# Kernel tuning notes

Hardware: AMD Instinct MI355X
Metric: run time of the kernel (lower is better)

The kernel has to match this reference:

```python
import jax, jax.numpy as jnp
import numpy as np

K = 5
K2 = K * K  # 25
SLOPE = 0.01  # torch leaky_relu default


def _unfold(x, k):
    # torch.nn.Unfold(k) on reflect-padded x: channel order c-major, then kh, kw
    b, c, h, w = x.shape
    p = k // 2
    xp = jnp.pad(x, ((0, 0), (0, 0), (p, p), (p, p)), mode='reflect')
    cols = jnp.stack([xp[:, :, i:i + h, j:j + w] for i in range(k) for j in range(k)], axis=2)
    return cols.reshape(b, c * k * k, h * w)  # (b, 3*k^2, h*w)


def _lin(x, W, b):
    # torch Linear: W is (out, in)
    return x @ W.T + b


def _lrelu(x):
    return jnp.where(x >= 0, x, SLOPE * x)


def setup_inputs() -> dict:
    key = jax.random.key(0)
    ks = iter(jax.random.split(key, 64))
    d = {}
    d['x'] = jax.random.uniform(next(ks), (4, 3, 384, 384), dtype=jnp.float32)

    def mk(name, out_f, in_f):
        d['W_' + name] = jax.random.normal(next(ks), (out_f, in_f), jnp.float32) * (1.0 / np.sqrt(in_f))
        d['b_' + name] = jax.random.normal(next(ks), (out_f,), jnp.float32) * 0.01

    mk('input', 2 * K2, 3 * K2)
    mk('h1', 3 * K2, 2 * K2)
    mk('h2', 3 * K2, 3 * K2)
    mk('h3', 2 * K2, 2 * K2)
    mk('h4', 5 * K2, 2 * K2)
    mk('h5', 2 * K2, 5 * K2)
    mk('out', 3, 2 * K2)
    # encoder(3*k^2): in -> 3*in -> in -> 3
    mk('e1', 9 * K2, 3 * K2); mk('e2', 3 * K2, 9 * K2); mk('e3', 3, 3 * K2)
    # encoder(2*k^2)
    mk('f1', 6 * K2, 2 * K2); mk('f2', 2 * K2, 6 * K2); mk('f3', 3, 2 * K2)
    # decoder(2*k^2): 3 -> out -> 3*out -> out
    mk('d1', 2 * K2, 3); mk('d2', 6 * K2, 2 * K2); mk('d3', 2 * K2, 6 * K2)
    return d


def reference(x,
              W_input, b_input, W_h1, b_h1, W_h2, b_h2, W_h3, b_h3,
              W_h4, b_h4, W_h5, b_h5, W_out, b_out,
              W_e1, b_e1, W_e2, b_e2, W_e3, b_e3,
              W_f1, b_f1, W_f2, b_f2, W_f3, b_f3,
              W_d1, b_d1, W_d2, b_d2, W_d3, b_d3):
    b, c, h, w = x.shape
    sw = jnp.transpose(_unfold(x, K), (0, 2, 1))  # (b, h*w, 3*k^2)
    x1 = _lin(sw, W_input, b_input)
    x2 = _lrelu(_lin(x1, W_h1, b_h1))
    x3 = jnp.tanh(_lin(x2, W_h2, b_h2))
    x3_enc = _lin(_lin(_lin(x3, W_e1, b_e1), W_e2, b_e2), W_e3, b_e3)
    enc2_x1 = _lin(_lin(_lin(x1, W_f1, b_f1), W_f2, b_f2), W_f3, b_f3)
    x4 = _lrelu(x3_enc + enc2_x1)
    x4_dec = _lin(_lin(_lin(_lin(x4, W_d1, b_d1), W_d2, b_d2), W_d3, b_d3), W_h3, b_h3)
    x5 = jnp.tanh(_lin(x4_dec, W_h4, b_h4))
    x6 = _lin(x5, W_h5, b_h5) - x1
    x7 = _lrelu(_lin(x6, W_out, b_out))  # (b, h*w, 3)
    return jnp.transpose(x7, (0, 2, 1)).reshape(b, c, h, w)
```

## Files before the change

### kernel.cpp

```cpp
#include <hip/hip_runtime.h>


#define IW 384
#define HW (384 * 384)
#define NPIX (4 * HW)
#define MTILE 128
#define NBLK (NPIX / MTILE)
#define NST 52
#define PT16 (16 * NST)

typedef _Float16 half8 __attribute__((ext_vector_type(8)));
typedef __fp16 fp16x2 __attribute__((ext_vector_type(2)));
typedef __attribute__((ext_vector_type(4))) float f32x4;
typedef __attribute__((ext_vector_type(2))) unsigned int uint2_;

#define MFMAH(A, B, C) __builtin_amdgcn_mfma_f32_16x16x32_f16((A), (B), (C), 0, 0, 0)

#define BA   0
#define B1   64
#define B2   144
#define BEF  224
#define BD   240
#define B4   304
#define B5   432
#define BOUT 496
#define BIAS_TOT 512

#define W_A0   0
#define W_A1   2048
#define W_A2   4096
#define W_H1A  6144
#define W_H1B  8704
#define W_H2A  11264
#define W_H2B  13824
#define W_H2C  16384
#define W_EF   18944
#define W_D    24064
#define W_H4C0 28160
#define W_H5C0 30208
#define W_OUT  44544
#define W_NI   45568
#define W_TOT  47616

#define STG_BE  24320
#define STG_BF  24336

__device__ __forceinline__ float lrelu(float v) { return fmaxf(v, 0.01f * v); }

#if __has_builtin(__builtin_amdgcn_exp2f)
#define EXP2F __builtin_amdgcn_exp2f
#else
#define EXP2F __builtin_exp2f
#endif

__device__ __forceinline__ float tanh_fast(float v) {
    float e = EXP2F(v * 2.8853900817779268f);
    return __builtin_fmaf(-2.0f, __builtin_amdgcn_rcpf(e + 1.0f), 1.0f);
}

__device__ __forceinline__ unsigned short f2h_bits(float v) {
    union { _Float16 h; unsigned short s; } u; u.h = (_Float16)v; return u.s;
}
__device__ __forceinline__ float h2f_bits(unsigned short s) {
    union { _Float16 h; unsigned short s; } u; u.s = s; return (float)u.h;
}
__device__ __forceinline__ unsigned packh2(float a, float b) {
    union { fp16x2 h; unsigned u; } u;
    u.h = __builtin_amdgcn_cvt_pkrtz(a, b);
    return u.u;
}

__device__ __forceinline__ void stage(float* dst, const float* __restrict__ src,
                                      int n, int tid) {
    int n4 = n >> 2;
    float4* d = (float4*)dst;
    const float4* s = (const float4*)src;
#pragma unroll 4
    for (int i = tid; i < n4; i += 256) d[i] = s[i];
    for (int i = (n4 << 2) + tid; i < n; i += 256) dst[i] = src[i];
}

__global__ __launch_bounds__(256) void setup_all(
    const float* __restrict__ W_input, const float* __restrict__ b_input,
    const float* __restrict__ W_h1,  const float* __restrict__ b_h1,
    const float* __restrict__ W_h2,  const float* __restrict__ b_h2,
    const float* __restrict__ W_h3,  const float* __restrict__ b_h3,
    const float* __restrict__ W_h4,  const float* __restrict__ b_h4,
    const float* __restrict__ W_h5,  const float* __restrict__ b_h5,
    const float* __restrict__ W_out, const float* __restrict__ b_out,
    const float* __restrict__ W_e1,  const float* __restrict__ b_e1,
    const float* __restrict__ W_e2,  const float* __restrict__ b_e2,
    const float* __restrict__ W_e3,  const float* __restrict__ b_e3,
    const float* __restrict__ W_f1,  const float* __restrict__ b_f1,
    const float* __restrict__ W_f2,  const float* __restrict__ b_f2,
    const float* __restrict__ W_f3,  const float* __restrict__ b_f3,
    const float* __restrict__ W_d1,  const float* __restrict__ b_d1,
    const float* __restrict__ W_d2,  const float* __restrict__ b_d2,
    const float* __restrict__ W_d3,  const float* __restrict__ b_d3,
    float* __restrict__ ws)
{
    const int tid = threadIdx.x;
    const int NT = 256;
    short* wimg = (short*)(ws + BIAS_TOT);

    if (blockIdx.x < 71) {
        const int soff[17] = {W_A0,W_A1,W_A2, W_H1A,W_H1B, W_H2A,W_H2B,W_H2C,
                              W_H4C0,W_H5C0, W_H4C0+4096,W_H5C0+4096,
                              W_H4C0+8192,W_H5C0+8192, W_H4C0+12288,W_H5C0+12288,
                              W_OUT};
        const int slay[17] = {0,0,0, 1,1, 2,2,2, 6,7, 6,7, 6,7, 6,7, 8};
        const int sNT[17]  = {4,4,4, 5,5, 5,5,5, 2,4, 2,4, 2,4, 2,4, 1};
        const int sKTS[17] = {1,1,1, 1,1, 1,1,1, 2,1, 2,1, 2,1, 2,1, 2};
        const int snb[17]  = {0,0,0, 0,0, 0,0,0, 0,0, 32,0, 64,0, 96,0, 0};
        const int skb[17]  = {0,32,64, 0,32, 0,32,64, 0,0, 0,32, 0,64, 0,96, 0};

        int seg = 0, local = blockIdx.x;
        while (seg < 16 && local >= sNT[seg] * sKTS[seg]) { local -= sNT[seg] * sKTS[seg]; seg++; }
        const int kts = sKTS[seg];
        const int kt = local % kts, nt = local / kts;
        const int lay = slay[seg];
        short* dst = wimg + soff[seg] + local * 512;

#pragma unroll
        for (int t = 0; t < 2; t++) {
            int idx = tid + t * 256;
            int j = idx & 7, lane = idx >> 3;
            int n = snb[seg] + nt * 16 + (lane & 15);
            int k = skb[seg] + kt * 32 + (lane >> 4) * 8 + j;
            float v = 0.0f;
            switch (lay) {
                case 0: if (n < 50  && k < 75)  v = W_input[n * 75 + k]; break;
                case 1: if (n < 75  && k < 50)  v = W_h1[n * 50 + k]; break;
                case 2: if (n < 75  && k < 75)  v = W_h2[n * 75 + k]; break;
                case 6: if (n < 125 && k < 50)  v = W_h4[n * 50 + k]; break;
                case 7: if (n < 50  && k < 125) v = W_h5[n * 125 + k]; break;
                case 8: if (n < 3   && k < 50)  v = W_out[n * 50 + k]; break;
            }
            dst[idx] = (short)f2h_bits(v);
        }
        return;
    }

    if (blockIdx.x == 74) {
        for (int i = tid; i < BIAS_TOT; i += NT) {
            if (i >= BD && i < B4) continue;
            float v = 0.0f;
            if (i < B1)        { int o = i - BA;   if (o < 50)  v = b_input[o]; }
            else if (i < B2)   { int o = i - B1;   if (o < 75)  v = b_h1[o]; }
            else if (i < BEF)  { int o = i - B2;   if (o < 75)  v = b_h2[o]; }
            else if (i < BD)   { v = 0.0f; }
            else if (i < B5)   { int o = i - B4;   if (o < 125) v = b_h4[o]; }
            else if (i < BOUT) { int o = i - B5;   if (o < 50)  v = b_h5[o]; }
            else               { int o = i - BOUT; if (o < 3)   v = b_out[o]; }
            ws[i] = v;
        }
        for (int i = tid; i < 2048; i += NT) {
            int j = i & 7, lane = (i >> 3) & 63, nt = i >> 9;
            int n = nt * 16 + (lane & 15);
            int k = (nt >> 1) * 32 + (lane >> 4) * 8 + j;
            wimg[W_NI + i] = (short)f2h_bits(k == n ? -1.0f : 0.0f);
        }
        return;
    }

    __shared__ __align__(16) float A[17500];
    __shared__ float B[675];
    __shared__ float C[256];
    __shared__ float Dd[256];
    __shared__ float Es[256];
    __shared__ float S[232];

    if (blockIdx.x == 71) {
        stage(A, W_e2, 16875, tid);
        for (int i = tid; i < 225; i += NT) { Es[i] = W_e3[i]; C[i] = b_e1[i]; }
        __syncthreads();
        for (int o = tid; o < 675; o += NT) {
            int r = o / 225, c = o % 225;
            float s0 = 0.f, s1 = 0.f, s2 = 0.f;
#pragma unroll
            for (int t = 0; t < 75; t += 3) {
                s0 += Es[r * 75 + t]     * A[t * 225 + c];
                s1 += Es[r * 75 + t + 1] * A[(t + 1) * 225 + c];
                s2 += Es[r * 75 + t + 2] * A[(t + 2) * 225 + c];
            }
            B[o] = s0 + s1 + s2;
        }
        for (int o = tid; o < 75; o += NT) {
            float s0 = 0.f, s1 = 0.f, s2 = 0.f;
#pragma unroll
            for (int t = 0; t < 225; t += 3) {
                s0 += A[o * 225 + t]     * C[t];
                s1 += A[o * 225 + t + 1] * C[t + 1];
                s2 += A[o * 225 + t + 2] * C[t + 2];
            }
            Dd[o] = b_e2[o] + s0 + s1 + s2;
        }
        __syncthreads();
        stage(A, W_e1, 16875, tid);
        __syncthreads();
        for (int o = tid; o < 225; o += NT) {
            int r = o / 75, c = o % 75;
            float s0 = 0.f, s1 = 0.f, s2 = 0.f;
#pragma unroll
            for (int t = 0; t < 225; t += 3) {
                s0 += B[r * 225 + t]     * A[t * 75 + c];
                s1 += B[r * 225 + t + 1] * A[(t + 1) * 75 + c];
                s2 += B[r * 225 + t + 2] * A[(t + 2) * 75 + c];
            }
            S[o] = s0 + s1 + s2;
        }
        for (int o = tid; o < 16; o += NT) {
            float s = 0.0f;
            if (o < 3) {
                s = b_e3[o];
                for (int t = 0; t < 75; t++) s += Es[o * 75 + t] * Dd[t];
            }
            ws[STG_BE + o] = s;
        }
        __syncthreads();
        for (int i = tid; i < 3072; i += NT) {
            int j = i & 7, lane = (i >> 3) & 63, frag = i >> 9, pl = frag & 1, kt = frag >> 1;
            int n = lane & 15, k = kt * 32 + (lane >> 4) * 8 + j;
            float v = (n < 3 && k < 75) ? S[n * 75 + k] : 0.0f;
            float hi = h2f_bits(f2h_bits(v));
            wimg[W_EF + i] = (short)(pl ? f2h_bits(v - hi) : f2h_bits(v));
        }
    } else if (blockIdx.x == 72) {
        stage(A,        W_f2, 7500, tid);
        stage(A + 7500, W_f1, 7500, tid);
        for (int i = tid; i < 150; i += NT) { Es[i] = W_f3[i]; C[i] = b_f1[i]; }
        __syncthreads();
        for (int o = tid; o < 450; o += NT) {
            int r = o / 150, c = o % 150;
            float s0 = 0.f, s1 = 0.f;
#pragma unroll
            for (int t = 0; t < 50; t += 2) {
                s0 += Es[r * 50 + t]     * A[t * 150 + c];
                s1 += Es[r * 50 + t + 1] * A[(t + 1) * 150 + c];
            }
            B[o] = s0 + s1;
        }
        for (int o = tid; o < 50; o += NT) {
            float s0 = 0.f, s1 = 0.f;
#pragma unroll
            for (int t = 0; t < 150; t += 2) {
                s0 += A[o * 150 + t]     * C[t];
                s1 += A[o * 150 + t + 1] * C[t + 1];
            }
            Dd[o] = b_f2[o] + s0 + s1;
        }
        __syncthreads();
        for (int o = tid; o < 150; o += NT) {
            int r = o / 50, c = o % 50;
            float s0 = 0.f, s1 = 0.f;
#pragma unroll
            for (int t = 0; t < 150; t += 2) {
                s0 += B[r * 150 + t]     * A[7500 + t * 50 + c];
                s1 += B[r * 150 + t + 1] * A[7500 + (t + 1) * 50 + c];
            }
            S[o] = s0 + s1;
        }
        for (int o = tid; o < 16; o += NT) {
            float s = 0.0f;
            if (o < 3) {
                s = b_f3[o];
                for (int t = 0; t < 50; t++) s += Es[o * 50 + t] * Dd[t];
            }
            ws[STG_BF + o] = s;
        }
        __syncthreads();
        for (int i = tid; i < 2048; i += NT) {
            int j = i & 7, lane = (i >> 3) & 63, frag = i >> 9, pl = frag & 1, kt = frag >> 1;
            int n = lane & 15, k = kt * 32 + (lane >> 4) * 8 + j;
            float v = (n < 3 && k < 50) ? S[n * 50 + k] : 0.0f;
            float hi = h2f_bits(f2h_bits(v));
            wimg[W_EF + 3072 + i] = (short)(pl ? f2h_bits(v - hi) : f2h_bits(v));
        }
    } else {
        stage(A,         W_d2, 7500, tid);
        stage(A + 7500,  W_d3, 7500, tid);
        stage(A + 15000, W_h3, 2500, tid);
        for (int i = tid; i < 150; i += NT) Es[i] = W_d1[i];
        for (int i = tid; i < 50;  i += NT) C[i] = b_d1[i];
        __syncthreads();
        for (int o = tid; o < 450; o += NT) {
            int r = o / 3, c = o % 3;
            float s0 = 0.f, s1 = 0.f;
#pragma unroll
            for (int t = 0; t < 50; t += 2) {
                s0 += A[r * 50 + t]     * Es[t * 3 + c];
                s1 += A[r * 50 + t + 1] * Es[(t + 1) * 3 + c];
            }
            B[o] = s0 + s1;
        }
        for (int o = tid; o < 150; o += NT) {
            float s0 = 0.f, s1 = 0.f;
#pragma unroll
            for (int t = 0; t < 50; t += 2) {
                s0 += A[o * 50 + t]     * C[t];
                s1 += A[o * 50 + t + 1] * C[t + 1];
            }
            Dd[o] = b_d2[o] + s0 + s1;
        }
        __syncthreads();
        for (int o = tid; o < 150; o += NT) {
            int r = o / 3, c = o % 3;
            float s0 = 0.f, s1 = 0.f;
#pragma unroll
            for (int t = 0; t < 150; t += 2) {
                s0 += A[7500 + r * 150 + t]     * B[t * 3 + c];
                s1 += A[7500 + r * 150 + t + 1] * B[(t + 1) * 3 + c];
            }
            Es[o] = s0 + s1;
        }
        for (int o = tid; o < 50; o += NT) {
            float s0 = 0.f, s1 = 0.f;
#pragma unroll
            for (int t = 0; t < 150; t += 2) {
                s0 += A[7500 + o * 150 + t]     * Dd[t];
                s1 += A[7500 + o * 150 + t + 1] * Dd[t + 1];
            }
            C[o] = b_d3[o] + s0 + s1;
        }
        __syncthreads();
        for (int o = tid; o < 150; o += NT) {
            int r = o / 3, c = o % 3;
            float s0 = 0.f, s1 = 0.f;
#pragma unroll
            for (int t = 0; t < 50; t += 2) {
                s0 += A[15000 + r * 50 + t]     * Es[t * 3 + c];
                s1 += A[15000 + r * 50 + t + 1] * Es[(t + 1) * 3 + c];
            }
            S[o] = s0 + s1;
        }
        for (int o = tid; o < 64; o += NT) {
            float v = 0.0f;
            if (o < 50) {
                float s0 = 0.f, s1 = 0.f;
#pragma unroll
                for (int t = 0; t < 50; t += 2) {
                    s0 += A[15000 + o * 50 + t]     * C[t];
                    s1 += A[15000 + o * 50 + t + 1] * C[t + 1];
                }
                v = b_h3[o] + s0 + s1;
            }
            ws[BD + o] = v;
        }
        __syncthreads();
        for (int i = tid; i < 4096; i += NT) {
            int j = i & 7, lane = (i >> 3) & 63, frag = i >> 9, pl = frag & 1, nt = frag >> 1;
            int n = nt * 16 + (lane & 15), k = (lane >> 4) * 8 + j;
            float v = (n < 50 && k < 3) ? S[n * 3 + k] : 0.0f;
            float hi = h2f_bits(f2h_bits(v));
            wimg[W_D + i] = (short)(pl ? f2h_bits(v - hi) : f2h_bits(v));
        }
    }
}

__device__ __forceinline__ half8 gfragH(const short* __restrict__ wl, int off) {
    return *(const half8*)(wl + off);
}

__device__ __forceinline__ void wB(unsigned int* p, f32x4 v) {
    uint2_ u;
    u[0] = packh2(v[0], v[1]);
    u[1] = packh2(v[2], v[3]);
    *(uint2_*)p = u;
}

__device__ __forceinline__ f32x4 lrelu4(f32x4 v) {
    v[0] = lrelu(v[0]); v[1] = lrelu(v[1]); v[2] = lrelu(v[2]); v[3] = lrelu(v[3]);
    return v;
}
__device__ __forceinline__ f32x4 tanh4(f32x4 v) {
    v[0] = tanh_fast(v[0]); v[1] = tanh_fast(v[1]);
    v[2] = tanh_fast(v[2]); v[3] = tanh_fast(v[3]);
    return v;
}

__global__ __launch_bounds__(256, 4) void fused_mfma(
    const float* __restrict__ xin,
    const float* __restrict__ ws,
    float* __restrict__ out)
{
    __shared__ unsigned int acts[MTILE * NST];

    const int tid = threadIdx.x;
    const int wv = tid >> 6;
    const int lane = tid & 63;
    const int qd = lane >> 4;
    const int mcol = lane & 15;
    const short* __restrict__ wl = (const short*)(ws + BIAS_TOT) + lane * 8;

    const int g0 = blockIdx.x * MTILE;
    const int bb = g0 / HW;
    const int p0 = g0 - bb * HW;
    const int yb = p0 / IW;
    const int xblk = p0 - yb * IW;
    const float* __restrict__ xb = xin + bb * 3 * HW;

    float* patch = (float*)acts;
    int*   stab  = (int*)(acts + 1984);

    for (int e = tid; e < 1980; e += 256) {
        int cr = e / 132;
        int i  = e - cr * 132;
        int c  = cr / 5, r = cr - c * 5;
        int ty = yb + r - 2; ty = ty < 0 ? -ty : ty; ty = (766 - ty) < ty ? 766 - ty : ty;
        int tx = xblk - 2 + i; tx = tx < 0 ? -tx : tx; tx = (766 - tx) < tx ? 766 - tx : tx;
        patch[cr * 132 + i] = xb[c * HW + ty * IW + tx];
    }
    if (tid < 96) {
        int v = 0;
        if (tid < 75) {
            int c = tid / 25, rem = tid - 25 * c;
            int rr = rem / 5, ss = rem - 5 * rr;
            v = (c * 5 + rr) * 132 + ss;
        }
        stab[tid] = v;
    }
    __syncthreads();

    half8 swf[3][2];
    {
        int st[3][8];
#pragma unroll
        for (int kt = 0; kt < 3; kt++)
#pragma unroll
            for (int j = 0; j < 8; j++)
                st[kt][j] = stab[kt * 32 + qd * 8 + j];
#pragma unroll
        for (int pt = 0; pt < 2; pt++) {
            const int xloc = wv * 32 + pt * 16 + mcol;
#pragma unroll
            for (int kt = 0; kt < 3; kt++) {
                union { unsigned u32[4]; half8 v; } u;
#pragma unroll
                for (int jj = 0; jj < 8; jj += 2) {
                    float v0 = patch[st[kt][jj]     + xloc];
                    float v1 = patch[st[kt][jj + 1] + xloc];
                    u.u32[jj >> 1] = packh2(v0, v1);
                }
                swf[kt][pt] = u.v;
            }
        }
    }
    __syncthreads();

    unsigned int* myrow = acts + (wv * 32 + mcol) * NST;
    unsigned int* wp = myrow + 2 * qd;
    const unsigned int* rp = myrow + 4 * qd;

    {
        uint2_ z; z[0] = 0u; z[1] = 0u;
        *(uint2_*)(wp + 40) = z;
        *(uint2_*)(wp + PT16 + 40) = z;
    }

    f32x4 accA[4][2];
#pragma unroll
    for (int mt = 0; mt < 4; mt++) {
        f32x4 b = *(const f32x4*)(ws + BA + mt * 16 + qd * 4);
        accA[mt][0] = b; accA[mt][1] = b;
    }
#pragma unroll
    for (int kt = 0; kt < 3; kt++)
#pragma unroll
        for (int mt = 0; mt < 4; mt++) {
            half8 w = gfragH(wl, W_A0 + kt * 2048 + mt * 512);
            accA[mt][0] = MFMAH(w, swf[kt][0], accA[mt][0]);
            accA[mt][1] = MFMAH(w, swf[kt][1], accA[mt][1]);
        }
#pragma unroll
    for (int mt = 0; mt < 4; mt++) {
        wB(wp + mt * 8,        accA[mt][0]);
        wB(wp + PT16 + mt * 8, accA[mt][1]);
    }
    half8 x1f[2][2];
#pragma unroll
    for (int kt = 0; kt < 2; kt++) {
        x1f[kt][0] = *(const half8*)(rp + kt * 16);
        x1f[kt][1] = *(const half8*)(rp + PT16 + kt * 16);
    }

    f32x4 acc1[5][2];
#pragma unroll
    for (int mt = 0; mt < 5; mt++) {
        f32x4 b = *(const f32x4*)(ws + B1 + mt * 16 + qd * 4);
        acc1[mt][0] = b; acc1[mt][1] = b;
    }
#pragma unroll
    for (int kt = 0; kt < 2; kt++)
#pragma unroll
        for (int mt = 0; mt < 5; mt++) {
            half8 w = gfragH(wl, W_H1A + kt * 2560 + mt * 512);
            acc1[mt][0] = MFMAH(w, x1f[kt][0], acc1[mt][0]);
            acc1[mt][1] = MFMAH(w, x1f[kt][1], acc1[mt][1]);
        }
#pragma unroll
    for (int mt = 0; mt < 5; mt++) {
        wB(wp + mt * 8,        lrelu4(acc1[mt][0]));
        wB(wp + PT16 + mt * 8, lrelu4(acc1[mt][1]));
    }

    f32x4 acc2[5][2];
#pragma unroll
    for (int mt = 0; mt < 5; mt++) {
        f32x4 b = *(const f32x4*)(ws + B2 + mt * 16 + qd * 4);
        acc2[mt][0] = b; acc2[mt][1] = b;
    }
#pragma unroll
    for (int kt = 0; kt < 3; kt++) {
        half8 a0 = *(const half8*)(rp + kt * 16);
        half8 a1 = *(const half8*)(rp + PT16 + kt * 16);
#pragma unroll
        for (int mt = 0; mt < 5; mt++) {
            half8 w = gfragH(wl, W_H2A + kt * 2560 + mt * 512);
            acc2[mt][0] = MFMAH(w, a0, acc2[mt][0]);
            acc2[mt][1] = MFMAH(w, a1, acc2[mt][1]);
        }
    }
#pragma unroll
    for (int mt = 0; mt < 5; mt++) {
        wB(wp + mt * 8,        tanh4(acc2[mt][0]));
        wB(wp + PT16 + mt * 8, tanh4(acc2[mt][1]));
    }

    f32x4 accEF[2];
    {
        f32x4 be = *(const f32x4*)(ws + STG_BE + qd * 4);
        f32x4 bf = *(const f32x4*)(ws + STG_BF + qd * 4);
        f32x4 b = be + bf;
        accEF[0] = b; accEF[1] = b;
    }
#pragma unroll
    for (int kt = 0; kt < 3; kt++) {
        half8 a0 = *(const half8*)(rp + kt * 16);
        half8 a1 = *(const half8*)(rp + PT16 + kt * 16);
        half8 wh = gfragH(wl, W_EF + kt * 1024);
        half8 wo = gfragH(wl, W_EF + kt * 1024 + 512);
        accEF[0] = MFMAH(wh, a0, accEF[0]); accEF[0] = MFMAH(wo, a0, accEF[0]);
        accEF[1] = MFMAH(wh, a1, accEF[1]); accEF[1] = MFMAH(wo, a1, accEF[1]);
    }
#pragma unroll
    for (int kt = 0; kt < 2; kt++) {
        half8 wh = gfragH(wl, W_EF + 3072 + kt * 1024);
        half8 wo = gfragH(wl, W_EF + 3072 + kt * 1024 + 512);
        accEF[0] = MFMAH(wh, x1f[kt][0], accEF[0]); accEF[0] = MFMAH(wo, x1f[kt][0], accEF[0]);
        accEF[1] = MFMAH(wh, x1f[kt][1], accEF[1]); accEF[1] = MFMAH(wo, x1f[kt][1], accEF[1]);
    }
    wB(wp,        lrelu4(accEF[0]));
    wB(wp + PT16, lrelu4(accEF[1]));

    half8 x4f[2];
    x4f[0] = *(const half8*)(rp);
    x4f[1] = *(const half8*)(rp + PT16);
    f32x4 accD[4][2];
#pragma unroll
    for (int mt = 0; mt < 4; mt++) {
        f32x4 b = *(const f32x4*)(ws + BD + mt * 16 + qd * 4);
        accD[mt][0] = b; accD[mt][1] = b;
    }
#pragma unroll
    for (int mt = 0; mt < 4; mt++) {
        half8 wh = gfragH(wl, W_D + mt * 1024);
        half8 wo = gfragH(wl, W_D + mt * 1024 + 512);
        accD[mt][0] = MFMAH(wh, x4f[0], accD[mt][0]); accD[mt][0] = MFMAH(wo, x4f[0], accD[mt][0]);
        accD[mt][1] = MFMAH(wh, x4f[1], accD[mt][1]); accD[mt][1] = MFMAH(wo, x4f[1], accD[mt][1]);
    }
#pragma unroll
    for (int mt = 0; mt < 4; mt++) {
        wB(wp + mt * 8,        accD[mt][0]);
        wB(wp + PT16 + mt * 8, accD[mt][1]);
    }
    half8 xdf[2][2];
#pragma unroll
    for (int kt = 0; kt < 2; kt++) {
        xdf[kt][0] = *(const half8*)(rp + kt * 16);
        xdf[kt][1] = *(const half8*)(rp + PT16 + kt * 16);
    }

    f32x4 x6a[4][2];
#pragma unroll
    for (int mt = 0; mt < 4; mt++) {
        f32x4 b = *(const f32x4*)(ws + B5 + mt * 16 + qd * 4);
        half8 nI = gfragH(wl, W_NI + mt * 512);
        x6a[mt][0] = MFMAH(nI, x1f[mt >> 1][0], b);
        x6a[mt][1] = MFMAH(nI, x1f[mt >> 1][1], b);
    }

#pragma unroll
    for (int c = 0; c < 4; c++) {
        const int slot = (c & 1) ? 16 : 32;
        f32x4 acc5[2][2];
#pragma unroll
        for (int mt2 = 0; mt2 < 2; mt2++) {
            f32x4 b = *(const f32x4*)(ws + B4 + c * 32 + mt2 * 16 + qd * 4);
            acc5[mt2][0] = b; acc5[mt2][1] = b;
        }
#pragma unroll
        for (int kt = 0; kt < 2; kt++)
#pragma unroll
            for (int mt2 = 0; mt2 < 2; mt2++) {
                half8 w = gfragH(wl, W_H4C0 + c * 4096 + (mt2 * 2 + kt) * 512);
                acc5[mt2][0] = MFMAH(w, xdf[kt][0], acc5[mt2][0]);
                acc5[mt2][1] = MFMAH(w, xdf[kt][1], acc5[mt2][1]);
            }
#pragma unroll
        for (int mt2 = 0; mt2 < 2; mt2++) {
            wB(wp + slot + mt2 * 8,        tanh4(acc5[mt2][0]));
            wB(wp + PT16 + slot + mt2 * 8, tanh4(acc5[mt2][1]));
        }
        half8 ch0 = *(const half8*)(rp + slot);
        half8 ch1 = *(const half8*)(rp + PT16 + slot);
#pragma unroll
        for (int mt = 0; mt < 4; mt++) {
            half8 w = gfragH(wl, W_H5C0 + c * 4096 + mt * 512);
            x6a[mt][0] = MFMAH(w, ch0, x6a[mt][0]);
            x6a[mt][1] = MFMAH(w, ch1, x6a[mt][1]);
        }
    }

#pragma unroll
    for (int mt = 0; mt < 4; mt++) {
        wB(wp + mt * 8,        x6a[mt][0]);
        wB(wp + PT16 + mt * 8, x6a[mt][1]);
    }
    f32x4 accO[2];
    {
        f32x4 b = *(const f32x4*)(ws + BOUT + qd * 4);
        accO[0] = b; accO[1] = b;
    }
#pragma unroll
    for (int kt = 0; kt < 2; kt++) {
        half8 a0 = *(const half8*)(rp + kt * 16);
        half8 a1 = *(const half8*)(rp + PT16 + kt * 16);
        half8 w = gfragH(wl, W_OUT + kt * 512);
        accO[0] = MFMAH(w, a0, accO[0]);
        accO[1] = MFMAH(w, a1, accO[1]);
    }
    if (qd == 0) {
#pragma unroll
        for (int pt = 0; pt < 2; pt++) {
            int p = p0 + wv * 32 + pt * 16 + mcol;
#pragma unroll
            for (int r = 0; r < 3; r++)
                out[(bb * 3 + r) * HW + p] = lrelu(accO[pt][r]);
        }
    }
}

extern "C" void kernel_launch(void* const* d_in, const int* in_sizes, int n_in,
                              void* d_out, int out_size, void* d_ws, size_t ws_size,
                              hipStream_t stream)
{
    const float* xin = (const float*)d_in[0];
    float* ws = (float*)d_ws;

    setup_all<<<75, 256, 0, stream>>>(
        (const float*)d_in[1],  (const float*)d_in[2],
        (const float*)d_in[3],  (const float*)d_in[4],
        (const float*)d_in[5],  (const float*)d_in[6],
        (const float*)d_in[7],  (const float*)d_in[8],
        (const float*)d_in[9],  (const float*)d_in[10],
        (const float*)d_in[11], (const float*)d_in[12],
        (const float*)d_in[13], (const float*)d_in[14],
        (const float*)d_in[15], (const float*)d_in[16],
        (const float*)d_in[17], (const float*)d_in[18],
        (const float*)d_in[19], (const float*)d_in[20],
        (const float*)d_in[21], (const float*)d_in[22],
        (const float*)d_in[23], (const float*)d_in[24],
        (const float*)d_in[25], (const float*)d_in[26],
        (const float*)d_in[27], (const float*)d_in[28],
        (const float*)d_in[29], (const float*)d_in[30],
        (const float*)d_in[31], (const float*)d_in[32],
        ws);

    fused_mfma<<<NBLK, 256, 0, stream>>>(xin, ws, (float*)d_out);
}
```

Baseline: 235.6 us.

## Chain MFMA layers in registers by permuting weight K-order instead of LDS round-trips

Stops writing each layer's fp16 activations to a shared-memory staging buffer and reading them back as B fragments. The weight images are prepacked with a permuted K ordering, so the MFMA accumulator output of one layer can be packed directly into the next layer's input fragment in registers. This removes LDS traffic and the associated waits between every layer and shrinks the shared allocation. In exchange it raises register pressure, and the out-of-range K lanes of the first layer now have to be zeroed explicitly.

```diff
diff --git a/kernel.cpp b/kernel.cpp
--- a/kernel.cpp
+++ b/kernel.cpp
@@ -6,13 +6,10 @@
 #define NPIX (4 * HW)
 #define MTILE 128
 #define NBLK (NPIX / MTILE)
-#define NST 52
-#define PT16 (16 * NST)
 
 typedef _Float16 half8 __attribute__((ext_vector_type(8)));
 typedef __fp16 fp16x2 __attribute__((ext_vector_type(2)));
 typedef __attribute__((ext_vector_type(4))) float f32x4;
-typedef __attribute__((ext_vector_type(2))) unsigned int uint2_;
 
 #define MFMAH(A, B, C) __builtin_amdgcn_mfma_f32_16x16x32_f16((A), (B), (C), 0, 0, 0)
 
@@ -125,8 +122,10 @@
         for (int t = 0; t < 2; t++) {
             int idx = tid + t * 256;
             int j = idx & 7, lane = idx >> 3;
+            int slot = (lay == 0) ? ((lane >> 4) * 8 + j)
+                                  : (4 * (lane >> 4) + (j & 3) + 16 * (j >> 2));
             int n = snb[seg] + nt * 16 + (lane & 15);
-            int k = skb[seg] + kt * 32 + (lane >> 4) * 8 + j;
+            int k = skb[seg] + kt * 32 + slot;
             float v = 0.0f;
             switch (lay) {
                 case 0: if (n < 50  && k < 75)  v = W_input[n * 75 + k]; break;
@@ -157,7 +156,7 @@
         for (int i = tid; i < 2048; i += NT) {
             int j = i & 7, lane = (i >> 3) & 63, nt = i >> 9;
             int n = nt * 16 + (lane & 15);
-            int k = (nt >> 1) * 32 + (lane >> 4) * 8 + j;
+            int k = (nt >> 1) * 32 + 4 * (lane >> 4) + (j & 3) + 16 * (j >> 2);
             wimg[W_NI + i] = (short)f2h_bits(k == n ? -1.0f : 0.0f);
         }
         return;
@@ -220,7 +219,8 @@
         __syncthreads();
         for (int i = tid; i < 3072; i += NT) {
             int j = i & 7, lane = (i >> 3) & 63, frag = i >> 9, pl = frag & 1, kt = frag >> 1;
-            int n = lane & 15, k = kt * 32 + (lane >> 4) * 8 + j;
+            int n = lane & 15;
+            int k = kt * 32 + 4 * (lane >> 4) + (j & 3) + 16 * (j >> 2);
             float v = (n < 3 && k < 75) ? S[n * 75 + k] : 0.0f;
             float hi = h2f_bits(f2h_bits(v));
             wimg[W_EF + i] = (short)(pl ? f2h_bits(v - hi) : f2h_bits(v));
@@ -271,7 +271,8 @@
         __syncthreads();
         for (int i = tid; i < 2048; i += NT) {
             int j = i & 7, lane = (i >> 3) & 63, frag = i >> 9, pl = frag & 1, kt = frag >> 1;
-            int n = lane & 15, k = kt * 32 + (lane >> 4) * 8 + j;
+            int n = lane & 15;
+            int k = kt * 32 + 4 * (lane >> 4) + (j & 3) + 16 * (j >> 2);
             float v = (n < 3 && k < 50) ? S[n * 50 + k] : 0.0f;
             float hi = h2f_bits(f2h_bits(v));
             wimg[W_EF + 3072 + i] = (short)(pl ? f2h_bits(v - hi) : f2h_bits(v));
@@ -349,7 +350,8 @@
         __syncthreads();
         for (int i = tid; i < 4096; i += NT) {
             int j = i & 7, lane = (i >> 3) & 63, frag = i >> 9, pl = frag & 1, nt = frag >> 1;
-            int n = nt * 16 + (lane & 15), k = (lane >> 4) * 8 + j;
+            int n = nt * 16 + (lane & 15);
+            int k = 4 * (lane >> 4) + (j & 3) + 16 * (j >> 2);
             float v = (n < 50 && k < 3) ? S[n * 3 + k] : 0.0f;
             float hi = h2f_bits(f2h_bits(v));
             wimg[W_D + i] = (short)(pl ? f2h_bits(v - hi) : f2h_bits(v));
@@ -361,11 +363,20 @@
     return *(const half8*)(wl + off);
 }
 
-__device__ __forceinline__ void wB(unsigned int* p, f32x4 v) {
-    uint2_ u;
-    u[0] = packh2(v[0], v[1]);
-    u[1] = packh2(v[2], v[3]);
-    *(uint2_*)p = u;
+__device__ __forceinline__ half8 packB(f32x4 lo, f32x4 hi) {
+    union { unsigned u32[4]; half8 v; } u;
+    u.u32[0] = packh2(lo[0], lo[1]);
+    u.u32[1] = packh2(lo[2], lo[3]);
+    u.u32[2] = packh2(hi[0], hi[1]);
+    u.u32[3] = packh2(hi[2], hi[3]);
+    return u.v;
+}
+__device__ __forceinline__ half8 packB1(f32x4 lo) {
+    union { unsigned u32[4]; half8 v; } u;
+    u.u32[0] = packh2(lo[0], lo[1]);
+    u.u32[1] = packh2(lo[2], lo[3]);
+    u.u32[2] = 0u; u.u32[3] = 0u;
+    return u.v;
 }
 
 __device__ __forceinline__ f32x4 lrelu4(f32x4 v) {
@@ -383,7 +394,8 @@
     const float* __restrict__ ws,
     float* __restrict__ out)
 {
-    __shared__ unsigned int acts[MTILE * NST];
+    __shared__ float patch[1984];
+    __shared__ int stab[96];
 
     const int tid = threadIdx.x;
     const int wv = tid >> 6;
@@ -398,9 +410,6 @@
     const int yb = p0 / IW;
     const int xblk = p0 - yb * IW;
     const float* __restrict__ xb = xin + bb * 3 * HW;
-
-    float* patch = (float*)acts;
-    int*   stab  = (int*)(acts + 1984);
 
     for (int e = tid; e < 1980; e += 256) {
         int cr = e / 132;
@@ -439,22 +448,16 @@
                 for (int jj = 0; jj < 8; jj += 2) {
                     float v0 = patch[st[kt][jj]     + xloc];
                     float v1 = patch[st[kt][jj + 1] + xloc];
+                    if (kt == 2) {
+                        int qq0 = 64 + qd * 8 + jj;
+                        v0 = (qq0     < 75) ? v0 : 0.0f;
+                        v1 = (qq0 + 1 < 75) ? v1 : 0.0f;
+                    }
                     u.u32[jj >> 1] = packh2(v0, v1);
                 }
                 swf[kt][pt] = u.v;
             }
         }
-    }
-    __syncthreads();
-
-    unsigned int* myrow = acts + (wv * 32 + mcol) * NST;
-    unsigned int* wp = myrow + 2 * qd;
-    const unsigned int* rp = myrow + 4 * qd;
-
-    {
-        uint2_ z; z[0] = 0u; z[1] = 0u;
-        *(uint2_*)(wp + 40) = z;
-        *(uint2_*)(wp + PT16 + 40) = z;
     }
 
     f32x4 accA[4][2];
@@ -471,17 +474,12 @@
             accA[mt][0] = MFMAH(w, swf[kt][0], accA[mt][0]);
             accA[mt][1] = MFMAH(w, swf[kt][1], accA[mt][1]);
         }
-#pragma unroll
-    for (int mt = 0; mt < 4; mt++) {
-        wB(wp + mt * 8,        accA[mt][0]);
-        wB(wp + PT16 + mt * 8, accA[mt][1]);
-    }
     half8 x1f[2][2];
 #pragma unroll
-    for (int kt = 0; kt < 2; kt++) {
-        x1f[kt][0] = *(const half8*)(rp + kt * 16);
-        x1f[kt][1] = *(const half8*)(rp + PT16 + kt * 16);
-    }
+    for (int kt = 0; kt < 2; kt++)
+#pragma unroll
+        for (int pt = 0; pt < 2; pt++)
+            x1f[kt][pt] = packB(accA[2 * kt][pt], accA[2 * kt + 1][pt]);
 
     f32x4 acc1[5][2];
 #pragma unroll
@@ -497,10 +495,12 @@
             acc1[mt][0] = MFMAH(w, x1f[kt][0], acc1[mt][0]);
             acc1[mt][1] = MFMAH(w, x1f[kt][1], acc1[mt][1]);
         }
-#pragma unroll
-    for (int mt = 0; mt < 5; mt++) {
-        wB(wp + mt * 8,        lrelu4(acc1[mt][0]));
-        wB(wp + PT16 + mt * 8, lrelu4(acc1[mt][1]));
+    half8 x2f[3][2];
+#pragma unroll
+    for (int pt = 0; pt < 2; pt++) {
+        x2f[0][pt] = packB (lrelu4(acc1[0][pt]), lrelu4(acc1[1][pt]));
+        x2f[1][pt] = packB (lrelu4(acc1[2][pt]), lrelu4(acc1[3][pt]));
+        x2f[2][pt] = packB1(lrelu4(acc1[4][pt]));
     }
 
     f32x4 acc2[5][2];
@@ -510,20 +510,19 @@
         acc2[mt][0] = b; acc2[mt][1] = b;
     }
 #pragma unroll
-    for (int kt = 0; kt < 3; kt++) {
-        half8 a0 = *(const half8*)(rp + kt * 16);
-        half8 a1 = *(const half8*)(rp + PT16 + kt * 16);
+    for (int kt = 0; kt < 3; kt++)
 #pragma unroll
         for (int mt = 0; mt < 5; mt++) {
             half8 w = gfragH(wl, W_H2A + kt * 2560 + mt * 512);
-            acc2[mt][0] = MFMAH(w, a0, acc2[mt][0]);
-            acc2[mt][1] = MFMAH(w, a1, acc2[mt][1]);
-        }
-    }
-#pragma unroll
-    for (int mt = 0; mt < 5; mt++) {
-        wB(wp + mt * 8,        tanh4(acc2[mt][0]));
-        wB(wp + PT16 + mt * 8, tanh4(acc2[mt][1]));
+            acc2[mt][0] = MFMAH(w, x2f[kt][0], acc2[mt][0]);
+            acc2[mt][1] = MFMAH(w, x2f[kt][1], acc2[mt][1]);
+        }
+    half8 x3f[3][2];
+#pragma unroll
+    for (int pt = 0; pt < 2; pt++) {
+        x3f[0][pt] = packB (tanh4(acc2[0][pt]), tanh4(acc2[1][pt]));
+        x3f[1][pt] = packB (tanh4(acc2[2][pt]), tanh4(acc2[3][pt]));
+        x3f[2][pt] = packB1(tanh4(acc2[4][pt]));
     }
 
     f32x4 accEF[2];
@@ -535,12 +534,10 @@
     }
 #pragma unroll
     for (int kt = 0; kt < 3; kt++) {
-        half8 a0 = *(const half8*)(rp + kt * 16);
-        half8 a1 = *(const half8*)(rp + PT16 + kt * 16);
         half8 wh = gfragH(wl, W_EF + kt * 1024);
         half8 wo = gfragH(wl, W_EF + kt * 1024 + 512);
-        accEF[0] = MFMAH(wh, a0, accEF[0]); accEF[0] = MFMAH(wo, a0, accEF[0]);
-        accEF[1] = MFMAH(wh, a1, accEF[1]); accEF[1] = MFMAH(wo, a1, accEF[1]);
+        accEF[0] = MFMAH(wh, x3f[kt][0], accEF[0]); accEF[0] = MFMAH(wo, x3f[kt][0], accEF[0]);
+        accEF[1] = MFMAH(wh, x3f[kt][1], accEF[1]); accEF[1] = MFMAH(wo, x3f[kt][1], accEF[1]);
     }
 #pragma unroll
     for (int kt = 0; kt < 2; kt++) {
@@ -549,12 +546,11 @@
         accEF[0] = MFMAH(wh, x1f[kt][0], accEF[0]); accEF[0] = MFMAH(wo, x1f[kt][0], accEF[0]);
         accEF[1] = MFMAH(wh, x1f[kt][1], accEF[1]); accEF[1] = MFMAH(wo, x1f[kt][1], accEF[1]);
     }
-    wB(wp,        lrelu4(accEF[0]));
-    wB(wp + PT16, lrelu4(accEF[1]));
-
     half8 x4f[2];
-    x4f[0] = *(const half8*)(rp);
-    x4f[1] = *(const half8*)(rp + PT16);
+#pragma unroll
+    for (int pt = 0; pt < 2; pt++)
+        x4f[pt] = packB1(lrelu4(accEF[pt]));
+
     f32x4 accD[4][2];
 #pragma unroll
     for (int mt = 0; mt < 4; mt++) {
@@ -568,17 +564,12 @@
         accD[mt][0] = MFMAH(wh, x4f[0], accD[mt][0]); accD[mt][0] = MFMAH(wo, x4f[0], accD[mt][0]);
         accD[mt][1] = MFMAH(wh, x4f[1], accD[mt][1]); accD[mt][1] = MFMAH(wo, x4f[1], accD[mt][1]);
     }
-#pragma unroll
-    for (int mt = 0; mt < 4; mt++) {
-        wB(wp + mt * 8,        accD[mt][0]);
-        wB(wp + PT16 + mt * 8, accD[mt][1]);
-    }
     half8 xdf[2][2];
 #pragma unroll
-    for (int kt = 0; kt < 2; kt++) {
-        xdf[kt][0] = *(const half8*)(rp + kt * 16);
-        xdf[kt][1] = *(const half8*)(rp + PT16 + kt * 16);
-    }
+    for (int kt = 0; kt < 2; kt++)
+#pragma unroll
+        for (int pt = 0; pt < 2; pt++)
+            xdf[kt][pt] = packB(accD[2 * kt][pt], accD[2 * kt + 1][pt]);
 
     f32x4 x6a[4][2];
 #pragma unroll
@@ -591,7 +582,6 @@
 
 #pragma unroll
     for (int c = 0; c < 4; c++) {
-        const int slot = (c & 1) ? 16 : 32;
         f32x4 acc5[2][2];
 #pragma unroll
         for (int mt2 = 0; mt2 < 2; mt2++) {
@@ -606,26 +596,18 @@
                 acc5[mt2][0] = MFMAH(w, xdf[kt][0], acc5[mt2][0]);
                 acc5[mt2][1] = MFMAH(w, xdf[kt][1], acc5[mt2][1]);
             }
-#pragma unroll
-        for (int mt2 = 0; mt2 < 2; mt2++) {
-            wB(wp + slot + mt2 * 8,        tanh4(acc5[mt2][0]));
-            wB(wp + PT16 + slot + mt2 * 8, tanh4(acc5[mt2][1]));
-        }
-        half8 ch0 = *(const half8*)(rp + slot);
-        half8 ch1 = *(const half8*)(rp + PT16 + slot);
+        half8 chf[2];
+#pragma unroll
+        for (int pt = 0; pt < 2; pt++)
+            chf[pt] = packB(tanh4(acc5[0][pt]), tanh4(acc5[1][pt]));
 #pragma unroll
         for (int mt = 0; mt < 4; mt++) {
             half8 w = gfragH(wl, W_H5C0 + c * 4096 + mt * 512);
-            x6a[mt][0] = MFMAH(w, ch0, x6a[mt][0]);
-            x6a[mt][1] = MFMAH(w, ch1, x6a[mt][1]);
-        }
-    }
-
-#pragma unroll
-    for (int mt = 0; mt < 4; mt++) {
-        wB(wp + mt * 8,        x6a[mt][0]);
-        wB(wp + PT16 + mt * 8, x6a[mt][1]);
-    }
+            x6a[mt][0] = MFMAH(w, chf[0], x6a[mt][0]);
+            x6a[mt][1] = MFMAH(w, chf[1], x6a[mt][1]);
+        }
+    }
+
     f32x4 accO[2];
     {
         f32x4 b = *(const f32x4*)(ws + BOUT + qd * 4);
@@ -633,11 +615,11 @@
     }
 #pragma unroll
     for (int kt = 0; kt < 2; kt++) {
-        half8 a0 = *(const half8*)(rp + kt * 16);
-        half8 a1 = *(const half8*)(rp + PT16 + kt * 16);
+        half8 x6f0 = packB(x6a[2 * kt][0], x6a[2 * kt + 1][0]);
+        half8 x6f1 = packB(x6a[2 * kt][1], x6a[2 * kt + 1][1]);
         half8 w = gfragH(wl, W_OUT + kt * 512);
-        accO[0] = MFMAH(w, a0, accO[0]);
-        accO[1] = MFMAH(w, a1, accO[1]);
+        accO[0] = MFMAH(w, x6f0, accO[0]);
+        accO[1] = MFMAH(w, x6f1, accO[1]);
     }
     if (qd == 0) {
 #pragma unroll
```

New measurement: 232.8 us. About the same (-1.2%).
